# Performance work log

Hardware: AMD Instinct MI355X
Metric: run time of the kernel (lower is better)

The kernel has to match this reference:

```python
import jax, jax.numpy as jnp
import numpy as np

VOCAB = 150
EOS = 2
PAD = 0
EPS = 1e-8


def _ngram_penalty_sum(tokens, n):
    # tokens: [B, S] int. Returns sum over batch of (count-2)*0.1*n for each
    # ngram repeated >=3 times. Equivalent trick: hash each ngram to a unique
    # int (base-VOCAB encoding), sort per row; a position is a 3rd-or-later
    # occurrence iff sorted[i] == sorted[i-2]; the number of such positions
    # equals sum over unique ngrams of max(count-2, 0).
    B, S = tokens.shape
    if S < n * 3:
        return jnp.float32(0.0)
    L = S - n + 1
    h = sum(tokens[:, j:j + L].astype(jnp.int32) * (VOCAB ** j) for j in range(n))
    hs = jnp.sort(h, axis=1)
    rep = jnp.sum(hs[:, 2:] == hs[:, :-2], axis=1)  # [B]
    return jnp.sum(rep.astype(jnp.float32)) * (0.1 * n)


def setup_inputs() -> dict:
    key = jax.random.key(0)
    k1, k2, k3 = jax.random.split(key, 3)
    B, S, V, IN = 256, 512, VOCAB, 512
    predictions = jax.random.normal(k1, (B, S, V), dtype=jnp.float32)
    targets = jax.random.randint(k2, (B, S), 0, V)
    attention_weights = jax.random.uniform(k3, (B, S, IN), dtype=jnp.float32)
    return {"predictions": predictions, "targets": targets,
            "attention_weights": attention_weights}


def reference(predictions, targets, attention_weights):
    B, S, V = predictions.shape

    # --- main NLL loss (ignore_index=PAD, mean over non-pad) ---
    mask = (targets != PAD).astype(predictions.dtype)  # [B,S]
    gathered = jnp.take_along_axis(predictions, targets[..., None], axis=-1)[..., 0]
    main = -jnp.sum(gathered * mask) / jnp.maximum(jnp.sum(mask), 1.0)

    # --- pattern penalty on argmax tokens ---
    pred_tokens = jnp.argmax(predictions, axis=-1)  # [B,S]
    pattern = (_ngram_penalty_sum(pred_tokens, 2)
               + _ngram_penalty_sum(pred_tokens, 3)
               + _ngram_penalty_sum(pred_tokens, 4)) / B

    # --- EOS encouragement ---
    eos_mask = (targets == EOS).astype(predictions.dtype)  # [B,S]
    eos_probs = jax.nn.softmax(predictions, axis=-1)[:, :, EOS]  # [B,S]
    eos_loss = -jnp.mean(eos_mask * jnp.log(eos_probs + EPS))
    eos_loss = jnp.where(jnp.sum(eos_mask) > 0, eos_loss, 0.0)
    has_eos_t = jnp.any(targets == EOS, axis=1)
    has_eos_p = jnp.any(pred_tokens == EOS, axis=1)
    no_eos = jnp.mean((has_eos_t & ~has_eos_p).astype(predictions.dtype))
    eos_total = eos_loss + 0.5 * no_eos

    # --- attention diversity (negative mean entropy, scaled) ---
    ent = -jnp.sum(attention_weights * jnp.log(attention_weights + EPS), axis=-1)
    attention = -jnp.mean(ent) * 0.1

    total = main + 0.1 * pattern + 0.2 * eos_total + 0.05 * attention
    return jnp.stack([total, main, pattern, eos_total, attention])
```

## Files before the change

kernel.cpp:

```cpp
#include <hip/hip_runtime.h>
#include <math.h>

#define BB   256
#define SS   512
#define VV   150
#define INW  512
#define NPOS (BB * SS)
#define GRID_A 1024
#define GRID_B 2048
#define EPSF 1e-8f


__global__ __launch_bounds__(256) void kern_ab(
    const float* __restrict__ pred, const int* __restrict__ tgt,
    const float* __restrict__ attw, float4* __restrict__ pA,
    float* __restrict__ pB, unsigned char* __restrict__ toks)
{
    __shared__ float shp[16];
    const int tid  = threadIdx.x;
    const int lane = tid & 63;
    const int wid  = tid >> 6;

    if (blockIdx.x < GRID_A) {
        const int gw = blockIdx.x * 4 + wid;
        float s_g = 0.f, s_mc = 0.f, s_el = 0.f, s_ec = 0.f;
        for (int it = 0; it < NPOS / (GRID_A * 4); ++it) {
            const int pos = gw + it * (GRID_A * 4);
            const float* row = pred + (size_t)pos * VV;
            const float v0 = row[lane];
            const float v1 = row[lane + 64];
            const bool  l3 = lane < (VV - 128);
            const float v2 = l3 ? row[lane + 128] : -INFINITY;

            float m = fmaxf(fmaxf(v0, v1), v2);
            #pragma unroll
            for (int off = 32; off > 0; off >>= 1)
                m = fmaxf(m, __shfl_xor(m, off));
            int li = (v0 == m) ? lane : (v1 == m) ? lane + 64
                     : (l3 && v2 == m) ? lane + 128 : (1 << 20);
            #pragma unroll
            for (int off = 32; off > 0; off >>= 1)
                li = min(li, __shfl_xor(li, off));

            const int t = tgt[pos];
            const float src = (t < 64) ? v0 : (t < 128) ? v1 : v2;
            const float g = __shfl(src, t & 63);

            if (t == 2) {
                float ex = __expf(v0 - m) + __expf(v1 - m)
                         + (l3 ? __expf(v2 - m) : 0.f);
                #pragma unroll
                for (int off = 32; off > 0; off >>= 1)
                    ex += __shfl_xor(ex, off);
                const float p2 = __shfl(v0, 2);
                if (lane == 0) {
                    s_el += __logf(__expf(p2 - m) / ex + EPSF);
                    s_ec += 1.f;
                }
            }
            if (lane == 0) {
                toks[pos] = (unsigned char)li;
                if (t != 0) { s_g += g; s_mc += 1.f; }
            }
        }
        if (lane == 0) {
            shp[wid * 4 + 0] = s_g;  shp[wid * 4 + 1] = s_mc;
            shp[wid * 4 + 2] = s_el; shp[wid * 4 + 3] = s_ec;
        }
        __syncthreads();
        if (tid == 0) {
            float4 r;
            r.x = shp[0] + shp[4] + shp[8]  + shp[12];
            r.y = shp[1] + shp[5] + shp[9]  + shp[13];
            r.z = shp[2] + shp[6] + shp[10] + shp[14];
            r.w = shp[3] + shp[7] + shp[11] + shp[15];
            pA[blockIdx.x] = r;
        }
    } else {
        const int bb = blockIdx.x - GRID_A;
        const float4* a4 = (const float4*)attw;
        const size_t stride = (size_t)GRID_B * 256;
        const size_t i0 = (size_t)bb * 256 + tid;
        float s = 0.f;
        #pragma unroll 4
        for (int it = 0; it < 32; ++it) {
            float4 v = a4[i0 + (size_t)it * stride];
            s += v.x * __logf(v.x + EPSF) + v.y * __logf(v.y + EPSF)
               + v.z * __logf(v.z + EPSF) + v.w * __logf(v.w + EPSF);
        }
        #pragma unroll
        for (int off = 32; off > 0; off >>= 1) s += __shfl_xor(s, off);
        if (lane == 0) shp[wid] = s;
        __syncthreads();
        if (tid == 0) pB[bb] = shp[0] + shp[1] + shp[2] + shp[3];
    }
}

__global__ __launch_bounds__(256) void kern_c(
    const unsigned char* __restrict__ toks, const int* __restrict__ tgt,
    int* __restrict__ pC, int* __restrict__ hasx)
{
    const int blk = blockIdx.x;
    const int b = blk & 255;
    const int n = 2 + (blk >> 8);
    const int L = SS - n + 1;

    __shared__ int tok[SS];
    __shared__ __align__(16) int h[SS];
    __shared__ int sflags;

    if (threadIdx.x == 0) sflags = 0;
    const unsigned char* rt = toks + b * SS;
    tok[threadIdx.x]       = rt[threadIdx.x];
    tok[threadIdx.x + 256] = rt[threadIdx.x + 256];
    __syncthreads();

    if (blk < 256) {
        const int* trow = tgt + b * SS;
        int f = 0;
        if (trow[threadIdx.x] == 2 || trow[threadIdx.x + 256] == 2) f |= 1;
        if (tok[threadIdx.x] == 2 || tok[threadIdx.x + 256] == 2)   f |= 2;
        if (f) atomicOr(&sflags, f);
    }

    #pragma unroll
    for (int q = 0; q < 2; ++q) {
        const int i = threadIdx.x + q * 256;
        int hv;
        if (i < L) {
            hv = tok[i];
            int mul = VV;
            for (int j = 1; j < n; ++j) { hv += tok[i + j] * mul; mul *= VV; }
        } else {
            hv = 0x7F000000 + i;
        }
        h[i] = hv;
    }
    __syncthreads();

    const int i1 = threadIdx.x, i2 = threadIdx.x + 256;
    const int h1 = h[i1], h2 = h[i2];
    int c1 = 0, c2 = 0;
    #pragma unroll 4
    for (int j = 0; j < SS; j += 4) {
        const int4 hv = *(const int4*)&h[j];
        c1 += (hv.x == h1 && j     < i1) + (hv.y == h1 && j + 1 < i1)
            + (hv.z == h1 && j + 2 < i1) + (hv.w == h1 && j + 3 < i1);
        c2 += (hv.x == h2 && j     < i2) + (hv.y == h2 && j + 1 < i2)
            + (hv.z == h2 && j + 2 < i2) + (hv.w == h2 && j + 3 < i2);
    }
    int rep = (c1 >= 2) + (c2 >= 2);
    #pragma unroll
    for (int off = 32; off > 0; off >>= 1) rep += __shfl_xor(rep, off);
    __shared__ int w4[4];
    if ((threadIdx.x & 63) == 0) w4[threadIdx.x >> 6] = rep;
    __syncthreads();
    if (threadIdx.x == 0) {
        pC[blk] = w4[0] + w4[1] + w4[2] + w4[3];
        if (blk < 256) hasx[b] = ((sflags & 1) && !(sflags & 2)) ? 1 : 0;
    }
}

__global__ __launch_bounds__(256) void kern_f(
    const int* __restrict__ hasx, const float4* __restrict__ pA,
    const float* __restrict__ pB, const int* __restrict__ pC,
    float* __restrict__ out)
{
    const int tid  = threadIdx.x;
    const int lane = tid & 63;
    const int wid  = tid >> 6;
    double v[9];
    #pragma unroll
    for (int k = 0; k < 9; ++k) v[k] = 0.0;

    for (int i = tid; i < GRID_A; i += 256) {
        const float4 p = pA[i];
        v[0] += p.x; v[1] += p.y; v[2] += p.z; v[3] += p.w;
    }
    for (int i = tid; i < GRID_B; i += 256) v[4] += pB[i];
    v[5] = pC[tid]; v[6] = pC[tid + 256]; v[7] = pC[tid + 512];
    v[8] = (double)hasx[tid];

    #pragma unroll
    for (int off = 32; off > 0; off >>= 1)
        #pragma unroll
        for (int k = 0; k < 9; ++k) v[k] += __shfl_xor(v[k], off);

    __shared__ double sd[4][9];
    if (lane == 0)
        for (int k = 0; k < 9; ++k) sd[wid][k] = v[k];
    __syncthreads();

    if (tid == 0) {
        double r[9];
        for (int k = 0; k < 9; ++k) r[k] = sd[0][k] + sd[1][k] + sd[2][k] + sd[3][k];
        const double mainv    = -r[0] / fmax(r[1], 1.0);
        const double eos_loss = (r[3] > 0.0) ? (-r[2] / (double)NPOS) : 0.0;
        const double no_eos   = r[8] / (double)BB;
        const double eos_tot  = eos_loss + 0.5 * no_eos;
        const double att      = 0.1 * r[4] / (double)NPOS;
        const double pattern  = (0.2 * r[5] + 0.3 * r[6] + 0.4 * r[7]) / (double)BB;
        const double total    = mainv + 0.1 * pattern + 0.2 * eos_tot + 0.05 * att;
        out[0] = (float)total;   out[1] = (float)mainv; out[2] = (float)pattern;
        out[3] = (float)eos_tot; out[4] = (float)att;
    }
}

extern "C" void kernel_launch(void* const* d_in, const int* in_sizes, int n_in,
                              void* d_out, int out_size, void* d_ws, size_t ws_size,
                              hipStream_t stream)
{
    const float* pred = (const float*)d_in[0];
    const int*   tgt  = (const int*)d_in[1];
    const float* attw = (const float*)d_in[2];
    float* out = (float*)d_out;
    char*  ws  = (char*)d_ws;

    float4* pA   = (float4*)ws;
    float*  pB   = (float*)(ws + 16384);
    int*    pC   = (int*)(ws + 24576);
    int*    hasx = (int*)(ws + 27648);
    unsigned char* toks = (unsigned char*)(ws + 28672);

    kern_ab<<<GRID_A + GRID_B, 256, 0, stream>>>(pred, tgt, attw, pA, pB, toks);
    kern_c<<<768, 256, 0, stream>>>(toks, tgt, pC, hasx);
    kern_f<<<1, 256, 0, stream>>>(hasx, pA, pB, pC, out);
}
```

Before: 112.2 us.

## Stage prediction rows through LDS with float4 loads and split attention kernel

The fused kernel is split into a prediction kernel and a separate attention-entropy kernel. The prediction kernel now loads 64 contiguous rows per block into shared memory with coalesced float4 loads, then has four threads per row compute the argmax, gather and softmax, replacing the one-row-per-wavefront scalar loads. This is meant to raise memory efficiency on the largest input, at the cost of about 38KB of LDS per block, which may limit occupancy, and one extra kernel launch that removes overlap between the two reductions.

```diff
diff --git a/kernel.cpp b/kernel.cpp
--- a/kernel.cpp
+++ b/kernel.cpp
@@ -6,94 +6,120 @@
 #define VV   150
 #define INW  512
 #define NPOS (BB * SS)
-#define GRID_A 1024
+#define GRID_A 2048
 #define GRID_B 2048
 #define EPSF 1e-8f
 
 
-__global__ __launch_bounds__(256) void kern_ab(
+__global__ __launch_bounds__(256) void kern_a(
     const float* __restrict__ pred, const int* __restrict__ tgt,
-    const float* __restrict__ attw, float4* __restrict__ pA,
-    float* __restrict__ pB, unsigned char* __restrict__ toks)
-{
+    float4* __restrict__ pA, unsigned char* __restrict__ toks)
+{
+    __shared__ __align__(16) float slab[64 * VV + 2];
     __shared__ float shp[16];
     const int tid  = threadIdx.x;
     const int lane = tid & 63;
     const int wid  = tid >> 6;
-
-    if (blockIdx.x < GRID_A) {
-        const int gw = blockIdx.x * 4 + wid;
-        float s_g = 0.f, s_mc = 0.f, s_el = 0.f, s_ec = 0.f;
-        for (int it = 0; it < NPOS / (GRID_A * 4); ++it) {
-            const int pos = gw + it * (GRID_A * 4);
-            const float* row = pred + (size_t)pos * VV;
-            const float v0 = row[lane];
-            const float v1 = row[lane + 64];
-            const bool  l3 = lane < (VV - 128);
-            const float v2 = l3 ? row[lane + 128] : -INFINITY;
-
-            float m = fmaxf(fmaxf(v0, v1), v2);
-            #pragma unroll
-            for (int off = 32; off > 0; off >>= 1)
-                m = fmaxf(m, __shfl_xor(m, off));
-            int li = (v0 == m) ? lane : (v1 == m) ? lane + 64
-                     : (l3 && v2 == m) ? lane + 128 : (1 << 20);
-            #pragma unroll
-            for (int off = 32; off > 0; off >>= 1)
-                li = min(li, __shfl_xor(li, off));
-
-            const int t = tgt[pos];
-            const float src = (t < 64) ? v0 : (t < 128) ? v1 : v2;
-            const float g = __shfl(src, t & 63);
-
-            if (t == 2) {
-                float ex = __expf(v0 - m) + __expf(v1 - m)
-                         + (l3 ? __expf(v2 - m) : 0.f);
-                #pragma unroll
-                for (int off = 32; off > 0; off >>= 1)
-                    ex += __shfl_xor(ex, off);
-                const float p2 = __shfl(v0, 2);
-                if (lane == 0) {
-                    s_el += __logf(__expf(p2 - m) / ex + EPSF);
-                    s_ec += 1.f;
-                }
-            }
-            if (lane == 0) {
-                toks[pos] = (unsigned char)li;
-                if (t != 0) { s_g += g; s_mc += 1.f; }
-            }
+    const int base = blockIdx.x * 64;
+
+    const float4* g4 = (const float4*)(pred + (size_t)base * VV);
+    float4* l4 = (float4*)slab;
+    #pragma unroll
+    for (int k = 0; k < 10; ++k) {
+        const int i = tid + k * 256;
+        if (i < 2400) l4[i] = g4[i];
+    }
+    __syncthreads();
+
+    const int p  = tid >> 2;
+    const int s  = tid & 3;
+    const int c0 = s * 38;
+    const float* row = slab + p * VV;
+    const float2* row2 = (const float2*)(row + c0);
+    const int t = tgt[base + p];
+
+    float m = -INFINITY; int mi = 200;
+    #pragma unroll
+    for (int j = 0; j < 19; ++j) {
+        const float2 v = row2[j];
+        const int c = c0 + 2 * j;
+        if (c     < VV && v.x > m) { m = v.x; mi = c; }
+        if (c + 1 < VV && v.y > m) { m = v.y; mi = c + 1; }
+    }
+    {
+        float om = __shfl_xor(m, 1); int oi = __shfl_xor(mi, 1);
+        if (om > m || (om == m && oi < mi)) { m = om; mi = oi; }
+        om = __shfl_xor(m, 2); oi = __shfl_xor(mi, 2);
+        if (om > m || (om == m && oi < mi)) { m = om; mi = oi; }
+    }
+
+    float acc_g = 0.f, acc_mc = 0.f, acc_el = 0.f, acc_ec = 0.f;
+    if (t != 0) {
+        if (s == t / 38) acc_g = row[t];
+        if (s == 0)      acc_mc = 1.f;
+    }
+    if (t == 2) {
+        float sx = 0.f;
+        #pragma unroll
+        for (int j = 0; j < 19; ++j) {
+            const float2 v = row2[j];
+            const int c = c0 + 2 * j;
+            if (c     < VV) sx += __expf(v.x - m);
+            if (c + 1 < VV) sx += __expf(v.y - m);
         }
-        if (lane == 0) {
-            shp[wid * 4 + 0] = s_g;  shp[wid * 4 + 1] = s_mc;
-            shp[wid * 4 + 2] = s_el; shp[wid * 4 + 3] = s_ec;
+        sx += __shfl_xor(sx, 1);
+        sx += __shfl_xor(sx, 2);
+        if (s == 0) {
+            acc_el = __logf(__expf(row[2] - m) / sx + EPSF);
+            acc_ec = 1.f;
         }
-        __syncthreads();
-        if (tid == 0) {
-            float4 r;
-            r.x = shp[0] + shp[4] + shp[8]  + shp[12];
-            r.y = shp[1] + shp[5] + shp[9]  + shp[13];
-            r.z = shp[2] + shp[6] + shp[10] + shp[14];
-            r.w = shp[3] + shp[7] + shp[11] + shp[15];
-            pA[blockIdx.x] = r;
-        }
-    } else {
-        const int bb = blockIdx.x - GRID_A;
-        const float4* a4 = (const float4*)attw;
-        const size_t stride = (size_t)GRID_B * 256;
-        const size_t i0 = (size_t)bb * 256 + tid;
-        float s = 0.f;
-        #pragma unroll 4
-        for (int it = 0; it < 32; ++it) {
-            float4 v = a4[i0 + (size_t)it * stride];
-            s += v.x * __logf(v.x + EPSF) + v.y * __logf(v.y + EPSF)
-               + v.z * __logf(v.z + EPSF) + v.w * __logf(v.w + EPSF);
-        }
-        #pragma unroll
-        for (int off = 32; off > 0; off >>= 1) s += __shfl_xor(s, off);
-        if (lane == 0) shp[wid] = s;
-        __syncthreads();
-        if (tid == 0) pB[bb] = shp[0] + shp[1] + shp[2] + shp[3];
-    }
+    }
+    if (s == 0) toks[base + p] = (unsigned char)mi;
+
+    #pragma unroll
+    for (int off = 32; off > 0; off >>= 1) {
+        acc_g  += __shfl_xor(acc_g,  off);
+        acc_mc += __shfl_xor(acc_mc, off);
+        acc_el += __shfl_xor(acc_el, off);
+        acc_ec += __shfl_xor(acc_ec, off);
+    }
+    if (lane == 0) {
+        shp[wid * 4 + 0] = acc_g;  shp[wid * 4 + 1] = acc_mc;
+        shp[wid * 4 + 2] = acc_el; shp[wid * 4 + 3] = acc_ec;
+    }
+    __syncthreads();
+    if (tid == 0) {
+        float4 r;
+        r.x = shp[0] + shp[4] + shp[8]  + shp[12];
+        r.y = shp[1] + shp[5] + shp[9]  + shp[13];
+        r.z = shp[2] + shp[6] + shp[10] + shp[14];
+        r.w = shp[3] + shp[7] + shp[11] + shp[15];
+        pA[blockIdx.x] = r;
+    }
+}
+
+__global__ __launch_bounds__(256) void kern_b(
+    const float* __restrict__ attw, float* __restrict__ pB)
+{
+    __shared__ float shp[4];
+    const int tid  = threadIdx.x;
+    const int lane = tid & 63;
+    const int wid  = tid >> 6;
+    const float4* a4 = (const float4*)attw;
+    const size_t stride = (size_t)GRID_B * 256;
+    const size_t i0 = (size_t)blockIdx.x * 256 + tid;
+    float s = 0.f;
+    #pragma unroll 8
+    for (int it = 0; it < 32; ++it) {
+        const float4 v = a4[i0 + (size_t)it * stride];
+        s += v.x * __logf(v.x + EPSF) + v.y * __logf(v.y + EPSF)
+           + v.z * __logf(v.z + EPSF) + v.w * __logf(v.w + EPSF);
+    }
+    #pragma unroll
+    for (int off = 32; off > 0; off >>= 1) s += __shfl_xor(s, off);
+    if (lane == 0) shp[wid] = s;
+    __syncthreads();
+    if (tid == 0) pB[blockIdx.x] = shp[0] + shp[1] + shp[2] + shp[3];
 }
 
 __global__ __launch_bounds__(256) void kern_c(
@@ -217,12 +243,13 @@
     char*  ws  = (char*)d_ws;
 
     float4* pA   = (float4*)ws;
-    float*  pB   = (float*)(ws + 16384);
-    int*    pC   = (int*)(ws + 24576);
-    int*    hasx = (int*)(ws + 27648);
-    unsigned char* toks = (unsigned char*)(ws + 28672);
-
-    kern_ab<<<GRID_A + GRID_B, 256, 0, stream>>>(pred, tgt, attw, pA, pB, toks);
+    float*  pB   = (float*)(ws + 32768);
+    int*    pC   = (int*)(ws + 40960);
+    int*    hasx = (int*)(ws + 44032);
+    unsigned char* toks = (unsigned char*)(ws + 45056);
+
+    kern_a<<<GRID_A, 256, 0, stream>>>(pred, tgt, pA, toks);
+    kern_b<<<GRID_B, 256, 0, stream>>>(attw, pB);
     kern_c<<<768, 256, 0, stream>>>(toks, tgt, pC, hasx);
     kern_f<<<1, 256, 0, stream>>>(hasx, pA, pB, pC, out);
 }
```

Result: faster. 108.2 us (-3.5%).

## Merge prediction and attention work per block, fold final reduction into last block

Applied to the files above, without the earlier changes.

Every block now handles both a slice of prediction rows and a slice of attention weights, replacing the earlier split into dedicated block groups. Attention loads switch to contiguous nontemporal vector loads. The separate single-block finalize kernel is removed: the last block of the n-gram kernel, identified through an atomic ticket counter, performs the final reduction. This saves one kernel launch and is meant to balance load across blocks, at the cost of a threadfence and atomic per block and a counter reset done inside the first kernel.

```diff
diff --git a/kernel.cpp b/kernel.cpp
--- a/kernel.cpp
+++ b/kernel.cpp
@@ -6,126 +6,131 @@
 #define VV   150
 #define INW  512
 #define NPOS (BB * SS)
-#define GRID_A 1024
-#define GRID_B 2048
+#define GRID 2048
 #define EPSF 1e-8f
+
+typedef float vf4 __attribute__((ext_vector_type(4)));
 
 
 __global__ __launch_bounds__(256) void kern_ab(
     const float* __restrict__ pred, const int* __restrict__ tgt,
     const float* __restrict__ attw, float4* __restrict__ pA,
-    float* __restrict__ pB, unsigned char* __restrict__ toks)
+    float* __restrict__ pB, unsigned char* __restrict__ toks,
+    int* __restrict__ counter)
 {
     __shared__ float shp[16];
+    __shared__ float shb[4];
     const int tid  = threadIdx.x;
     const int lane = tid & 63;
     const int wid  = tid >> 6;
 
-    if (blockIdx.x < GRID_A) {
-        const int gw = blockIdx.x * 4 + wid;
-        float s_g = 0.f, s_mc = 0.f, s_el = 0.f, s_ec = 0.f;
-        for (int it = 0; it < NPOS / (GRID_A * 4); ++it) {
-            const int pos = gw + it * (GRID_A * 4);
-            const float* row = pred + (size_t)pos * VV;
-            const float v0 = row[lane];
-            const float v1 = row[lane + 64];
-            const bool  l3 = lane < (VV - 128);
-            const float v2 = l3 ? row[lane + 128] : -INFINITY;
-
-            float m = fmaxf(fmaxf(v0, v1), v2);
+    if (blockIdx.x == 0 && tid == 0) *counter = 0;
+
+    const int gw = blockIdx.x * 4 + wid;
+    float s_g = 0.f, s_mc = 0.f, s_el = 0.f, s_ec = 0.f;
+    for (int it = 0; it < 16; ++it) {
+        const int pos = gw + it * 8192;
+        const float* row = pred + (size_t)pos * VV;
+        const float v0 = row[lane];
+        const float v1 = row[lane + 64];
+        const bool  l3 = lane < (VV - 128);
+        const float v2 = l3 ? row[lane + 128] : -INFINITY;
+
+        float m = fmaxf(fmaxf(v0, v1), v2);
+        #pragma unroll
+        for (int off = 32; off > 0; off >>= 1)
+            m = fmaxf(m, __shfl_xor(m, off));
+        int li = (v0 == m) ? lane : (v1 == m) ? lane + 64
+                 : (l3 && v2 == m) ? lane + 128 : (1 << 20);
+        #pragma unroll
+        for (int off = 32; off > 0; off >>= 1)
+            li = min(li, __shfl_xor(li, off));
+
+        const int t = tgt[pos];
+        const float src = (t < 64) ? v0 : (t < 128) ? v1 : v2;
+        const float g = __shfl(src, t & 63);
+
+        if (t == 2) {
+            float ex = __expf(v0 - m) + __expf(v1 - m)
+                     + (l3 ? __expf(v2 - m) : 0.f);
             #pragma unroll
             for (int off = 32; off > 0; off >>= 1)
-                m = fmaxf(m, __shfl_xor(m, off));
-            int li = (v0 == m) ? lane : (v1 == m) ? lane + 64
-                     : (l3 && v2 == m) ? lane + 128 : (1 << 20);
-            #pragma unroll
-            for (int off = 32; off > 0; off >>= 1)
-                li = min(li, __shfl_xor(li, off));
-
-            const int t = tgt[pos];
-            const float src = (t < 64) ? v0 : (t < 128) ? v1 : v2;
-            const float g = __shfl(src, t & 63);
-
-            if (t == 2) {
-                float ex = __expf(v0 - m) + __expf(v1 - m)
-                         + (l3 ? __expf(v2 - m) : 0.f);
-                #pragma unroll
-                for (int off = 32; off > 0; off >>= 1)
-                    ex += __shfl_xor(ex, off);
-                const float p2 = __shfl(v0, 2);
-                if (lane == 0) {
-                    s_el += __logf(__expf(p2 - m) / ex + EPSF);
-                    s_ec += 1.f;
-                }
-            }
+                ex += __shfl_xor(ex, off);
+            const float p2 = __shfl(v0, 2);
             if (lane == 0) {
-                toks[pos] = (unsigned char)li;
-                if (t != 0) { s_g += g; s_mc += 1.f; }
+                s_el += __logf(__expf(p2 - m) / ex + EPSF);
+                s_ec += 1.f;
             }
         }
         if (lane == 0) {
-            shp[wid * 4 + 0] = s_g;  shp[wid * 4 + 1] = s_mc;
-            shp[wid * 4 + 2] = s_el; shp[wid * 4 + 3] = s_ec;
+            toks[pos] = (unsigned char)li;
+            if (t != 0) { s_g += g; s_mc += 1.f; }
         }
-        __syncthreads();
-        if (tid == 0) {
-            float4 r;
-            r.x = shp[0] + shp[4] + shp[8]  + shp[12];
-            r.y = shp[1] + shp[5] + shp[9]  + shp[13];
-            r.z = shp[2] + shp[6] + shp[10] + shp[14];
-            r.w = shp[3] + shp[7] + shp[11] + shp[15];
-            pA[blockIdx.x] = r;
-        }
-    } else {
-        const int bb = blockIdx.x - GRID_A;
-        const float4* a4 = (const float4*)attw;
-        const size_t stride = (size_t)GRID_B * 256;
-        const size_t i0 = (size_t)bb * 256 + tid;
-        float s = 0.f;
-        #pragma unroll 4
-        for (int it = 0; it < 32; ++it) {
-            float4 v = a4[i0 + (size_t)it * stride];
-            s += v.x * __logf(v.x + EPSF) + v.y * __logf(v.y + EPSF)
-               + v.z * __logf(v.z + EPSF) + v.w * __logf(v.w + EPSF);
-        }
-        #pragma unroll
-        for (int off = 32; off > 0; off >>= 1) s += __shfl_xor(s, off);
-        if (lane == 0) shp[wid] = s;
-        __syncthreads();
-        if (tid == 0) pB[bb] = shp[0] + shp[1] + shp[2] + shp[3];
+    }
+    if (lane == 0) {
+        shp[wid * 4 + 0] = s_g;  shp[wid * 4 + 1] = s_mc;
+        shp[wid * 4 + 2] = s_el; shp[wid * 4 + 3] = s_ec;
+    }
+
+    const vf4* a4 = (const vf4*)attw;
+    const size_t base = (size_t)blockIdx.x * 8192;
+    float s = 0.f;
+    #pragma unroll 8
+    for (int it = 0; it < 32; ++it) {
+        const vf4 v = __builtin_nontemporal_load(a4 + base + it * 256 + tid);
+        s += v.x * __logf(v.x + EPSF) + v.y * __logf(v.y + EPSF)
+           + v.z * __logf(v.z + EPSF) + v.w * __logf(v.w + EPSF);
+    }
+    #pragma unroll
+    for (int off = 32; off > 0; off >>= 1) s += __shfl_xor(s, off);
+    if (lane == 0) shb[wid] = s;
+
+    __syncthreads();
+    if (tid == 0) {
+        float4 r;
+        r.x = shp[0] + shp[4] + shp[8]  + shp[12];
+        r.y = shp[1] + shp[5] + shp[9]  + shp[13];
+        r.z = shp[2] + shp[6] + shp[10] + shp[14];
+        r.w = shp[3] + shp[7] + shp[11] + shp[15];
+        pA[blockIdx.x] = r;
+        pB[blockIdx.x] = shb[0] + shb[1] + shb[2] + shb[3];
     }
 }
 
-__global__ __launch_bounds__(256) void kern_c(
+__global__ __launch_bounds__(256) void kern_cf(
     const unsigned char* __restrict__ toks, const int* __restrict__ tgt,
-    int* __restrict__ pC, int* __restrict__ hasx)
+    int* __restrict__ pC, int* __restrict__ hasx, int* __restrict__ counter,
+    const float4* __restrict__ pA, const float* __restrict__ pB,
+    float* __restrict__ out)
 {
     const int blk = blockIdx.x;
     const int b = blk & 255;
     const int n = 2 + (blk >> 8);
     const int L = SS - n + 1;
+    const int tid = threadIdx.x;
 
     __shared__ int tok[SS];
     __shared__ __align__(16) int h[SS];
     __shared__ int sflags;
-
-    if (threadIdx.x == 0) sflags = 0;
+    __shared__ int sticket;
+
+    if (tid == 0) sflags = 0;
     const unsigned char* rt = toks + b * SS;
-    tok[threadIdx.x]       = rt[threadIdx.x];
-    tok[threadIdx.x + 256] = rt[threadIdx.x + 256];
+    tok[tid]       = rt[tid];
+    tok[tid + 256] = rt[tid + 256];
     __syncthreads();
 
     if (blk < 256) {
         const int* trow = tgt + b * SS;
         int f = 0;
-        if (trow[threadIdx.x] == 2 || trow[threadIdx.x + 256] == 2) f |= 1;
-        if (tok[threadIdx.x] == 2 || tok[threadIdx.x + 256] == 2)   f |= 2;
+        if (trow[tid] == 2 || trow[tid + 256] == 2) f |= 1;
+        if (tok[tid] == 2 || tok[tid + 256] == 2)   f |= 2;
         if (f) atomicOr(&sflags, f);
     }
 
     #pragma unroll
     for (int q = 0; q < 2; ++q) {
-        const int i = threadIdx.x + q * 256;
+        const int i = tid + q * 256;
         int hv;
         if (i < L) {
             hv = tok[i];
@@ -138,7 +143,7 @@
     }
     __syncthreads();
 
-    const int i1 = threadIdx.x, i2 = threadIdx.x + 256;
+    const int i1 = tid, i2 = tid + 256;
     const int h1 = h[i1], h2 = h[i2];
     int c1 = 0, c2 = 0;
     #pragma unroll 4
@@ -153,31 +158,28 @@
     #pragma unroll
     for (int off = 32; off > 0; off >>= 1) rep += __shfl_xor(rep, off);
     __shared__ int w4[4];
-    if ((threadIdx.x & 63) == 0) w4[threadIdx.x >> 6] = rep;
-    __syncthreads();
-    if (threadIdx.x == 0) {
+    if ((tid & 63) == 0) w4[tid >> 6] = rep;
+    __syncthreads();
+    if (tid == 0) {
         pC[blk] = w4[0] + w4[1] + w4[2] + w4[3];
         if (blk < 256) hasx[b] = ((sflags & 1) && !(sflags & 2)) ? 1 : 0;
-    }
-}
-
-__global__ __launch_bounds__(256) void kern_f(
-    const int* __restrict__ hasx, const float4* __restrict__ pA,
-    const float* __restrict__ pB, const int* __restrict__ pC,
-    float* __restrict__ out)
-{
-    const int tid  = threadIdx.x;
+        __threadfence();
+        sticket = atomicAdd(counter, 1);
+    }
+    __syncthreads();
+    if (sticket != 768 - 1) return;
+
+    __threadfence();
     const int lane = tid & 63;
     const int wid  = tid >> 6;
     double v[9];
     #pragma unroll
     for (int k = 0; k < 9; ++k) v[k] = 0.0;
-
-    for (int i = tid; i < GRID_A; i += 256) {
+    for (int i = tid; i < GRID; i += 256) {
         const float4 p = pA[i];
         v[0] += p.x; v[1] += p.y; v[2] += p.z; v[3] += p.w;
     }
-    for (int i = tid; i < GRID_B; i += 256) v[4] += pB[i];
+    for (int i = tid; i < GRID; i += 256) v[4] += pB[i];
     v[5] = pC[tid]; v[6] = pC[tid + 256]; v[7] = pC[tid + 512];
     v[8] = (double)hasx[tid];
 
@@ -217,12 +219,12 @@
     char*  ws  = (char*)d_ws;
 
     float4* pA   = (float4*)ws;
-    float*  pB   = (float*)(ws + 16384);
-    int*    pC   = (int*)(ws + 24576);
-    int*    hasx = (int*)(ws + 27648);
-    unsigned char* toks = (unsigned char*)(ws + 28672);
-
-    kern_ab<<<GRID_A + GRID_B, 256, 0, stream>>>(pred, tgt, attw, pA, pB, toks);
-    kern_c<<<768, 256, 0, stream>>>(toks, tgt, pC, hasx);
-    kern_f<<<1, 256, 0, stream>>>(hasx, pA, pB, pC, out);
+    float*  pB   = (float*)(ws + 32768);
+    int*    pC   = (int*)(ws + 40960);
+    int*    hasx = (int*)(ws + 44032);
+    int*    cnt  = (int*)(ws + 45056);
+    unsigned char* toks = (unsigned char*)(ws + 45312);
+
+    kern_ab<<<GRID, 256, 0, stream>>>(pred, tgt, attw, pA, pB, toks, cnt);
+    kern_cf<<<768, 256, 0, stream>>>(toks, tgt, pC, hasx, cnt, pA, pB, out);
 }
```

Measured after the change: 100.6 us. 10.3% less time.
